# Kernel optimization log

Hardware: AMD Instinct MI355X
Metric: run time of the kernel (lower is better)

## Reference

```python
import jax, jax.numpy as jnp
import numpy as np

T, B, I, H = 512, 64, 512, 512

def setup_inputs() -> dict:
    key = jax.random.key(0)
    k1, k2, k3 = jax.random.split(key, 3)
    # scale weights to keep tanh out of deep saturation
    return {
        "input": jax.random.normal(k1, (T, B, I), dtype=jnp.float32),
        "w_ih": jax.random.normal(k2, (H, I), dtype=jnp.float32) / np.sqrt(I),
        "w_hh": jax.random.normal(k3, (H, H), dtype=jnp.float32) / np.sqrt(H),
    }

def reference(input, w_ih, w_hh):
    # vanilla tanh RNN: h_t = tanh(x_t @ w_ih^T + h_{t-1} @ w_hh^T)
    batch = input.shape[1]
    h0 = jnp.zeros((batch, w_hh.shape[0]), dtype=input.dtype)

    def step(h_prev, x):
        h = jnp.tanh(x @ w_ih.T + h_prev @ w_hh.T)
        return h, h

    h_last, h_all = jax.lax.scan(step, h0, input)
    return h_all, h_last
```

## Files before the change

### kernel.cpp

```cpp
#include <hip/hip_runtime.h>
#include <cmath>

#define T_STEPS 512
#define BATCH   64
#define ISZ     512
#define HSZ     512
#define EXN     32768

__global__ __launch_bounds__(256) void rnn_xw_f32(const float* __restrict__ x,
                                                  const float* __restrict__ wih,
                                                  float* __restrict__ out) {
    __shared__ float As[32][68];
    __shared__ float Bs[32][68];

    const int tid = threadIdx.x;
    const int n0  = blockIdx.x * 64;
    const int m0  = blockIdx.y * 64;
    const int r0  = (tid & 15) * 4;
    const int c0  = (tid >> 4) * 4;
    const int sr  = tid >> 2;
    const int sc  = (tid & 3) * 8;

    float acc[4][4] = {};

    const float* ap = x   + (size_t)(m0 + sr) * ISZ + sc;
    const float* bp = wih + (size_t)(n0 + sr) * ISZ + sc;

    for (int k0 = 0; k0 < ISZ; k0 += 32) {
        const float4 a0 = *(const float4*)(ap + k0);
        const float4 a1 = *(const float4*)(ap + k0 + 4);
        const float4 b0 = *(const float4*)(bp + k0);
        const float4 b1 = *(const float4*)(bp + k0 + 4);
        __syncthreads();
        As[sc + 0][sr] = a0.x; As[sc + 1][sr] = a0.y;
        As[sc + 2][sr] = a0.z; As[sc + 3][sr] = a0.w;
        As[sc + 4][sr] = a1.x; As[sc + 5][sr] = a1.y;
        As[sc + 6][sr] = a1.z; As[sc + 7][sr] = a1.w;
        Bs[sc + 0][sr] = b0.x; Bs[sc + 1][sr] = b0.y;
        Bs[sc + 2][sr] = b0.z; Bs[sc + 3][sr] = b0.w;
        Bs[sc + 4][sr] = b1.x; Bs[sc + 5][sr] = b1.y;
        Bs[sc + 6][sr] = b1.z; Bs[sc + 7][sr] = b1.w;
        __syncthreads();

        #pragma unroll
        for (int k = 0; k < 32; ++k) {
            const float4 av = *(const float4*)&As[k][r0];
            const float4 bv = *(const float4*)&Bs[k][c0];
            const float a[4] = {av.x, av.y, av.z, av.w};
            const float b[4] = {bv.x, bv.y, bv.z, bv.w};
            #pragma unroll
            for (int i = 0; i < 4; ++i)
                #pragma unroll
                for (int j = 0; j < 4; ++j)
                    acc[i][j] = fmaf(a[i], b[j], acc[i][j]);
        }
    }

    #pragma unroll
    for (int i = 0; i < 4; ++i) {
        float4 v; v.x = acc[i][0]; v.y = acc[i][1]; v.z = acc[i][2]; v.w = acc[i][3];
        *(float4*)(out + (size_t)(m0 + r0 + i) * HSZ + n0 + c0) = v;
    }
}

__device__ __forceinline__ void ex_store(unsigned long long* w, float h, unsigned tag) {
    union { float f; unsigned u; } c; c.f = h;
    const unsigned long long v = ((unsigned long long)tag << 32) | (unsigned long long)c.u;
    __hip_atomic_store(w, v, __ATOMIC_RELAXED, __HIP_MEMORY_SCOPE_AGENT);
}

__global__ __launch_bounds__(512, 2) void rnn_rec(const float* __restrict__ whh,
                                                  float* __restrict__ out,
                                                  unsigned long long* __restrict__ ex) {
    __shared__ float hl[1024];
    __shared__ float red[1024];
    float4* hl4 = (float4*)hl;

    const int tid  = threadIdx.x;
    const int p    = blockIdx.x >> 3;
    const int g    = blockIdx.x & 7;
    const int j0   = g * 64;
    const int b    = tid & 1;
    const int jg   = (tid >> 1) & 15;
    const int kseg = tid >> 5;
    const int lane = tid & 63;
    const int wv   = tid >> 6;

    float4 w[4][8];
    #pragma unroll
    for (int jx = 0; jx < 4; ++jx) {
        const float* wr = whh + (size_t)(j0 + jg * 4 + jx) * HSZ + kseg * 32;
        #pragma unroll
        for (int i = 0; i < 8; ++i)
            w[jx][i] = *(const float4*)(wr + 4 * i);
    }

    const int fb = tid & 1;
    const int fj = (tid >> 1) & 63;

    unsigned long long* exw0 = ex + (size_t)(2 * p + 0) * 512 + tid;
    unsigned long long* exw1 = ex + (size_t)(2 * p + 1) * 512 + tid;

    for (int t = 0; t < T_STEPS; ++t) {
        float xwv = 0.f;
        if (tid < 128)
            xwv = out[((size_t)t * BATCH + 2 * p + fb) * HSZ + j0 + fj];

        float acc = 0.f;
        if (t > 0) {
            const size_t soff = (size_t)((t - 1) & 1) * EXN;
            unsigned long long v0 = __hip_atomic_load(exw0 + soff, __ATOMIC_RELAXED,
                                                      __HIP_MEMORY_SCOPE_AGENT);
            unsigned long long v1 = __hip_atomic_load(exw1 + soff, __ATOMIC_RELAXED,
                                                      __HIP_MEMORY_SCOPE_AGENT);
            while ((unsigned)(v0 >> 32) != (unsigned)t ||
                   (unsigned)(v1 >> 32) != (unsigned)t) {
                __builtin_amdgcn_s_sleep(1);
                v0 = __hip_atomic_load(exw0 + soff, __ATOMIC_RELAXED,
                                       __HIP_MEMORY_SCOPE_AGENT);
                v1 = __hip_atomic_load(exw1 + soff, __ATOMIC_RELAXED,
                                       __HIP_MEMORY_SCOPE_AGENT);
            }
            union { unsigned u; float f; } c0, c1;
            c0.u = (unsigned)v0; c1.u = (unsigned)v1;
            hl[tid]       = c0.f;
            hl[512 + tid] = c1.f;
            __syncthreads();

            float p4[4] = {0.f, 0.f, 0.f, 0.f};
            #pragma unroll
            for (int i = 0; i < 8; ++i) {
                const float4 h4 = hl4[b * 128 + kseg * 8 + i];
                #pragma unroll
                for (int jx = 0; jx < 4; ++jx) {
                    p4[jx] = fmaf(w[jx][i].x, h4.x, p4[jx]);
                    p4[jx] = fmaf(w[jx][i].y, h4.y, p4[jx]);
                    p4[jx] = fmaf(w[jx][i].z, h4.z, p4[jx]);
                    p4[jx] = fmaf(w[jx][i].w, h4.w, p4[jx]);
                }
            }
            #pragma unroll
            for (int jx = 0; jx < 4; ++jx)
                p4[jx] += __shfl_xor(p4[jx], 32, 64);
            if (lane < 32) {
                float4 v; v.x = p4[0]; v.y = p4[1]; v.z = p4[2]; v.w = p4[3];
                *(float4*)&red[(wv * 32 + lane) * 4] = v;
            }
            __syncthreads();
            if (tid < 128) {
                const int c = (fj >> 2) * 2 + fb;
                const int ji = fj & 3;
                #pragma unroll
                for (int w8 = 0; w8 < 8; ++w8)
                    acc += red[(w8 * 32 + c) * 4 + ji];
            }
        }

        if (tid < 128) {
            const float a2 = acc + xwv;
            const float e  = __expf(2.f * a2);
            const float hv = 1.f - 2.f / (e + 1.f);
            out[((size_t)t * BATCH + 2 * p + fb) * HSZ + j0 + fj] = hv;
            if (t < T_STEPS - 1)
                ex_store(ex + (size_t)(t & 1) * EXN + (size_t)(2 * p + fb) * 512 + j0 + fj,
                         hv, (unsigned)(t + 1));
            else
                out[(size_t)T_STEPS * BATCH * HSZ + (size_t)(2 * p + fb) * HSZ + j0 + fj] = hv;
        }
    }
}

extern "C" void kernel_launch(void* const* d_in, const int* in_sizes, int n_in,
                              void* d_out, int out_size, void* d_ws, size_t ws_size,
                              hipStream_t stream) {
    (void)in_sizes; (void)n_in; (void)out_size; (void)ws_size;
    const float* x    = (const float*)d_in[0];
    const float* wih  = (const float*)d_in[1];
    const float* whh  = (const float*)d_in[2];
    float*       out  = (float*)d_out;
    unsigned long long* ex = (unsigned long long*)d_ws;

    (void)hipMemsetAsync(d_ws, 0, 2 * EXN * sizeof(unsigned long long), stream);

    hipLaunchKernelGGL(rnn_xw_f32, dim3(8, 512), dim3(256), 0, stream, x, wih, out);
    hipLaunchKernelGGL(rnn_rec, dim3(256), dim3(512), 0, stream, whh, out, ex);
}
```

Before: 1.140 ms.

## Reduce recurrence partial sums by wave shuffles, drop second barrier per step

Reassigns the recurrent matvec so each wave owns 8 output neurons for both batch rows, with lanes splitting K. The cross-segment reduction becomes an in-wave xor-shuffle tree instead of an LDS scratch buffer plus a second __syncthreads. The hidden-state LDS buffer is double-buffered by parity and padded to avoid bank conflicts. Outputs and exchange stores are written by lanes 0-1 of each wave as vectorised 8-wide chunks. The cost is more shuffle instructions and fewer lanes doing the tanh and the stores.

```diff
diff --git a/kernel.cpp b/kernel.cpp
--- a/kernel.cpp
+++ b/kernel.cpp
@@ -72,100 +72,110 @@
 __global__ __launch_bounds__(512, 2) void rnn_rec(const float* __restrict__ whh,
                                                   float* __restrict__ out,
                                                   unsigned long long* __restrict__ ex) {
-    __shared__ float hl[1024];
-    __shared__ float red[1024];
-    float4* hl4 = (float4*)hl;
+    __shared__ float4 hl4[660];
+    float* hl = (float*)hl4;
 
     const int tid  = threadIdx.x;
     const int p    = blockIdx.x >> 3;
     const int g    = blockIdx.x & 7;
     const int j0   = g * 64;
-    const int b    = tid & 1;
-    const int jg   = (tid >> 1) & 15;
-    const int kseg = tid >> 5;
     const int lane = tid & 63;
     const int wv   = tid >> 6;
+    const int b    = lane & 1;
+    const int ks   = lane >> 1;
 
-    float4 w[4][8];
+    float4 wq[32];
+    {
+        const float* wr = whh + (size_t)(j0 + wv * 8) * HSZ + ks * 16;
+        #pragma unroll
+        for (int jx = 0; jx < 8; ++jx)
+            #pragma unroll
+            for (int i = 0; i < 4; ++i)
+                wq[jx * 4 + i] = *(const float4*)(wr + (size_t)jx * HSZ + 4 * i);
+    }
     #pragma unroll
-    for (int jx = 0; jx < 4; ++jx) {
-        const float* wr = whh + (size_t)(j0 + jg * 4 + jx) * HSZ + kseg * 32;
-        #pragma unroll
-        for (int i = 0; i < 8; ++i)
-            w[jx][i] = *(const float4*)(wr + 4 * i);
-    }
+    for (int n = 0; n < 32; ++n)
+        asm volatile("" : "+v"(wq[n].x), "+v"(wq[n].y), "+v"(wq[n].z), "+v"(wq[n].w));
 
-    const int fb = tid & 1;
-    const int fj = (tid >> 1) & 63;
-
-    unsigned long long* exw0 = ex + (size_t)(2 * p + 0) * 512 + tid;
-    unsigned long long* exw1 = ex + (size_t)(2 * p + 1) * 512 + tid;
+    unsigned long long* exb = ex + (size_t)(2 * p) * 512 + tid;
+    const int fo = (((tid >> 4) * 5 + ((tid >> 2) & 3)) << 2) + (tid & 3);
 
     for (int t = 0; t < T_STEPS; ++t) {
-        float xwv = 0.f;
-        if (tid < 128)
-            xwv = out[((size_t)t * BATCH + 2 * p + fb) * HSZ + j0 + fj];
+        float4 xwa, xwb;
+        if (lane < 2) {
+            const float* xp = out + ((size_t)t * BATCH + 2 * p + lane) * HSZ + j0 + wv * 8;
+            xwa = *(const float4*)xp;
+            xwb = *(const float4*)(xp + 4);
+        }
 
-        float acc = 0.f;
+        float p8[8] = {0.f, 0.f, 0.f, 0.f, 0.f, 0.f, 0.f, 0.f};
         if (t > 0) {
-            const size_t soff = (size_t)((t - 1) & 1) * EXN;
-            unsigned long long v0 = __hip_atomic_load(exw0 + soff, __ATOMIC_RELAXED,
+            const int    s    = (t - 1) & 1;
+            const size_t soff = (size_t)s * EXN;
+            unsigned long long v0 = __hip_atomic_load(exb + soff, __ATOMIC_RELAXED,
                                                       __HIP_MEMORY_SCOPE_AGENT);
-            unsigned long long v1 = __hip_atomic_load(exw1 + soff, __ATOMIC_RELAXED,
+            unsigned long long v1 = __hip_atomic_load(exb + soff + 512, __ATOMIC_RELAXED,
                                                       __HIP_MEMORY_SCOPE_AGENT);
             while ((unsigned)(v0 >> 32) != (unsigned)t ||
                    (unsigned)(v1 >> 32) != (unsigned)t) {
                 __builtin_amdgcn_s_sleep(1);
-                v0 = __hip_atomic_load(exw0 + soff, __ATOMIC_RELAXED,
+                v0 = __hip_atomic_load(exb + soff, __ATOMIC_RELAXED,
                                        __HIP_MEMORY_SCOPE_AGENT);
-                v1 = __hip_atomic_load(exw1 + soff, __ATOMIC_RELAXED,
+                v1 = __hip_atomic_load(exb + soff + 512, __ATOMIC_RELAXED,
                                        __HIP_MEMORY_SCOPE_AGENT);
             }
             union { unsigned u; float f; } c0, c1;
             c0.u = (unsigned)v0; c1.u = (unsigned)v1;
-            hl[tid]       = c0.f;
-            hl[512 + tid] = c1.f;
+            hl[s * 1320 + fo]       = c0.f;
+            hl[s * 1320 + 660 + fo] = c1.f;
             __syncthreads();
 
-            float p4[4] = {0.f, 0.f, 0.f, 0.f};
+            const float4* hb = hl4 + s * 330 + b * 165 + ks * 5;
             #pragma unroll
-            for (int i = 0; i < 8; ++i) {
-                const float4 h4 = hl4[b * 128 + kseg * 8 + i];
+            for (int i = 0; i < 4; ++i) {
+                const float4 h4 = hb[i];
                 #pragma unroll
-                for (int jx = 0; jx < 4; ++jx) {
-                    p4[jx] = fmaf(w[jx][i].x, h4.x, p4[jx]);
-                    p4[jx] = fmaf(w[jx][i].y, h4.y, p4[jx]);
-                    p4[jx] = fmaf(w[jx][i].z, h4.z, p4[jx]);
-                    p4[jx] = fmaf(w[jx][i].w, h4.w, p4[jx]);
+                for (int jx = 0; jx < 8; ++jx) {
+                    const float4 wv4 = wq[jx * 4 + i];
+                    p8[jx] = fmaf(wv4.x, h4.x, p8[jx]);
+                    p8[jx] = fmaf(wv4.y, h4.y, p8[jx]);
+                    p8[jx] = fmaf(wv4.z, h4.z, p8[jx]);
+                    p8[jx] = fmaf(wv4.w, h4.w, p8[jx]);
                 }
             }
             #pragma unroll
-            for (int jx = 0; jx < 4; ++jx)
-                p4[jx] += __shfl_xor(p4[jx], 32, 64);
-            if (lane < 32) {
-                float4 v; v.x = p4[0]; v.y = p4[1]; v.z = p4[2]; v.w = p4[3];
-                *(float4*)&red[(wv * 32 + lane) * 4] = v;
-            }
-            __syncthreads();
-            if (tid < 128) {
-                const int c = (fj >> 2) * 2 + fb;
-                const int ji = fj & 3;
+            for (int d = 2; d <= 32; d <<= 1)
                 #pragma unroll
-                for (int w8 = 0; w8 < 8; ++w8)
-                    acc += red[(w8 * 32 + c) * 4 + ji];
-            }
+                for (int jx = 0; jx < 8; ++jx)
+                    p8[jx] += __shfl_xor(p8[jx], d, 64);
         }
 
-        if (tid < 128) {
-            const float a2 = acc + xwv;
-            const float e  = __expf(2.f * a2);
-            const float hv = 1.f - 2.f / (e + 1.f);
-            out[((size_t)t * BATCH + 2 * p + fb) * HSZ + j0 + fj] = hv;
-            if (t < T_STEPS - 1)
-                ex_store(ex + (size_t)(t & 1) * EXN + (size_t)(2 * p + fb) * 512 + j0 + fj,
-                         hv, (unsigned)(t + 1));
-            else
-                out[(size_t)T_STEPS * BATCH * HSZ + (size_t)(2 * p + fb) * HSZ + j0 + fj] = hv;
+        if (lane < 2) {
+            float hv[8];
+            #pragma unroll
+            for (int n = 0; n < 8; ++n) {
+                const float a2 = p8[n] + ((n < 4) ? (&xwa.x)[n] : (&xwb.x)[n - 4]);
+                const float e  = __expf(2.f * a2);
+                hv[n] = 1.f - 2.f / (e + 1.f);
+            }
+            float* op = out + ((size_t)t * BATCH + 2 * p + lane) * HSZ + j0 + wv * 8;
+            float4 o0, o1;
+            o0.x = hv[0]; o0.y = hv[1]; o0.z = hv[2]; o0.w = hv[3];
+            o1.x = hv[4]; o1.y = hv[5]; o1.z = hv[6]; o1.w = hv[7];
+            *(float4*)op       = o0;
+            *(float4*)(op + 4) = o1;
+            if (t < T_STEPS - 1) {
+                unsigned long long* ep = ex + (size_t)(t & 1) * EXN
+                                       + (size_t)(2 * p + lane) * 512 + j0 + wv * 8;
+                #pragma unroll
+                for (int n = 0; n < 8; ++n)
+                    ex_store(ep + n, hv[n], (unsigned)(t + 1));
+            } else {
+                float* lp = out + (size_t)T_STEPS * BATCH * HSZ
+                          + (size_t)(2 * p + lane) * HSZ + j0 + wv * 8;
+                *(float4*)lp       = o0;
+                *(float4*)(lp + 4) = o1;
+            }
         }
     }
 }
```

Result: slower. 2.493 ms (+118.6%).
